# Kernel tuning notes

Measured on AMD Instinct MI355X. Metric: run time of the kernel, lower is better.

Reference implementation:

```python
import jax, jax.numpy as jnp
import numpy as np

MARGIN = 0.3
EPS = 1e-6      # torch F.pairwise_distance eps used inside TripletMarginLoss
BIG = 1000000.0  # same sentinel as original code


def setup_inputs() -> dict:
    key = jax.random.key(0)
    k1, k2 = jax.random.split(key)
    embeddings = jax.random.normal(k1, (4096, 2048), dtype=jnp.float32)
    labels = jax.random.randint(k2, (4096,), 0, 128)  # 128 identities -> ~32 samples each
    return {"embeddings": embeddings, "labels": labels}


def _batch_hard_triplet_loss(emb, labels):
    B = emb.shape[0]
    # pairwise euclidean distances (torch.cdist p=2)
    sq = jnp.sum(emb * emb, axis=1)                      # [B]
    d2 = sq[:, None] + sq[None, :] - 2.0 * (emb @ emb.T)  # [B,B]
    dists = jnp.sqrt(jnp.maximum(d2, 0.0))

    same = labels[:, None] == labels[None, :]            # [B,B] bool
    eye = jnp.eye(B, dtype=bool)
    pos_mask = same & ~eye

    # hard positive: argmax over same-label (self set to -1, others-with-diff-label masked to 0*d -> use -1 uniformly for non-positives, matching dists*mask_pos with diag=-1 since dists>=0)
    pos_d = jnp.where(pos_mask, dists, -1.0)
    hard_pos = jnp.argmax(pos_d, axis=1)                 # [B]
    # hard negative: argmin over different-label (same-label gets +1e6 like original)
    neg_d = jnp.where(same, dists + BIG, dists)
    hard_neg = jnp.argmin(neg_d, axis=1)                 # [B]

    # valid anchors: at least one positive (other than self) and one negative
    valid = (jnp.sum(pos_mask, axis=1) > 0) & (jnp.sum(~same, axis=1) > 0)

    # TripletMarginLoss recomputes distances with eps added to the difference
    dp = jnp.linalg.norm(emb - emb[hard_pos] + EPS, axis=1)
    dn = jnp.linalg.norm(emb - emb[hard_neg] + EPS, axis=1)
    per = jnp.maximum(dp - dn + MARGIN, 0.0)

    cnt = jnp.sum(valid)
    total = jnp.sum(jnp.where(valid, per, 0.0))
    return jnp.where(cnt > 0, total / jnp.maximum(cnt, 1).astype(per.dtype), 0.0)


def reference(embeddings, labels):
    return _batch_hard_triplet_loss(embeddings, labels)
```

## Files before the change

### kernel.cpp

```cpp
#include <hip/hip_runtime.h>
#include <stdint.h>

#define B 4096
#define D 2048
#define BK 128
#define NITER (D / BK)
#define BM 64
#define BN 128

typedef unsigned long long ull;
typedef float f32x4 __attribute__((ext_vector_type(4)));
typedef long v2l __attribute__((ext_vector_type(2)));

#define SENT_P 0x00000000FFFFFFFFull
#define SENT_N (~0ull)

__device__ __forceinline__ void async_copy16(const unsigned char* g, unsigned char* l) {
  __builtin_amdgcn_global_load_lds(
      (const __attribute__((address_space(1))) unsigned int*)g,
      (__attribute__((address_space(3))) unsigned int*)l,
      16, 0, 0);
}

__global__ void k_convert_sq(const float* __restrict__ emb,
                             unsigned char* __restrict__ embq,
                             float* __restrict__ sq,
                             float* __restrict__ rs,
                             ull* __restrict__ bp,
                             ull* __restrict__ bn) {
  const int row = blockIdx.x, t = threadIdx.x;
  const float4* src = (const float4*)(emb + (size_t)row * D);
  float4 v0 = src[2 * t], v1 = src[2 * t + 1];
  float s = v0.x * v0.x + v0.y * v0.y + v0.z * v0.z + v0.w * v0.w
          + v1.x * v1.x + v1.y * v1.y + v1.z * v1.z + v1.w * v1.w;
  float sm = v0.x + v0.y + v0.z + v0.w + v1.x + v1.y + v1.z + v1.w;

  unsigned w0 = __builtin_amdgcn_cvt_pk_fp8_f32(v0.x, v0.y, 0, false);
  w0 = __builtin_amdgcn_cvt_pk_fp8_f32(v0.z, v0.w, w0, true);
  unsigned w1 = __builtin_amdgcn_cvt_pk_fp8_f32(v1.x, v1.y, 0, false);
  w1 = __builtin_amdgcn_cvt_pk_fp8_f32(v1.z, v1.w, w1, true);
  uint2 o; o.x = w0; o.y = w1;
  const int pos = ((t >> 4) << 7) | ((t & 3) << 5) | (((t >> 2) & 3) << 3);
  *(uint2*)(embq + (size_t)row * D + pos) = o;

  for (int off = 32; off; off >>= 1) {
    s  += __shfl_down(s, off, 64);
    sm += __shfl_down(sm, off, 64);
  }
  __shared__ float ps[4], pm[4];
  int lane = t & 63, wave = t >> 6;
  if (lane == 0) { ps[wave] = s; pm[wave] = sm; }
  __syncthreads();
  if (t == 0) {
    sq[row] = ps[0] + ps[1] + ps[2] + ps[3];
    rs[row] = pm[0] + pm[1] + pm[2] + pm[3];
    bp[row] = SENT_P;
    bn[row] = SENT_N;
  }
}

__launch_bounds__(256, 4)
__global__ void k_gemm_select(const unsigned char* __restrict__ embq,
                              const float* __restrict__ sq,
                              const int* __restrict__ labels,
                              ull* __restrict__ best_pos,
                              ull* __restrict__ best_neg) {
  __shared__ __align__(16) unsigned char ldsA[BM * BK];
  __shared__ __align__(16) unsigned char ldsB[BN * BK];

  int rem = blockIdx.x, p = 0;
  while (rem >= 2 * (32 - p)) { rem -= 2 * (32 - p); ++p; }
  int by = 2 * p;
  int c = 32 - p;
  if (rem >= c) { by += 1; rem -= c; }
  const int bx = p + rem;

  const int tid  = threadIdx.x;
  const int lane = tid & 63;
  const int wave = tid >> 6;
  const int wm = wave >> 1, wn = wave & 1;
  const int q = lane >> 4, m15 = lane & 15;
  const int ibase = by * BM, jbase = bx * BN;

  int aoff[2][2], boff[2][4];
#pragma unroll
  for (int sh = 0; sh < 2; ++sh) {
#pragma unroll
    for (int g = 0; g < 2; ++g) {
      int ra = wm * 32 + g * 16 + m15;
      aoff[sh][g] = ra * BK + (((q * 2 + sh) ^ (ra & 7)) * 16);
    }
#pragma unroll
    for (int g = 0; g < 4; ++g) {
      int rb = wn * 64 + g * 16 + m15;
      boff[sh][g] = rb * BK + (((q * 2 + sh) ^ (rb & 7)) * 16);
    }
  }

  const int srow = lane >> 3;
  const int slot = lane & 7;
  size_t agoff[2], bgoff[4];
  int lasta[2], lastb[4];
#pragma unroll
  for (int pp = 0; pp < 2; ++pp) {
    int r0  = wave * 16 + pp * 8;
    int row = r0 + srow;
    agoff[pp] = (size_t)(ibase + row) * D + (slot ^ (row & 7)) * 16;
    lasta[pp] = r0 * BK;
  }
#pragma unroll
  for (int pp = 0; pp < 4; ++pp) {
    int r0  = wave * 32 + pp * 8;
    int row = r0 + srow;
    bgoff[pp] = (size_t)(jbase + row) * D + (slot ^ (row & 7)) * 16;
    lastb[pp] = r0 * BK;
  }

  f32x4 acc[2][4];
  const f32x4 z = {0.f, 0.f, 0.f, 0.f};
#pragma unroll
  for (int a = 0; a < 2; ++a)
#pragma unroll
    for (int b = 0; b < 4; ++b) acc[a][b] = z;

  for (int kb = 0; kb < D; kb += BK) {
    __syncthreads();
#pragma unroll
    for (int pp = 0; pp < 2; ++pp)
      async_copy16(embq + agoff[pp] + kb, &ldsA[lasta[pp]]);
#pragma unroll
    for (int pp = 0; pp < 4; ++pp)
      async_copy16(embq + bgoff[pp] + kb, &ldsB[lastb[pp]]);
    __syncthreads();

#pragma unroll
    for (int sh = 0; sh < 2; ++sh) {
      v2l af[2], bf[4];
#pragma unroll
      for (int g = 0; g < 2; ++g) af[g] = *(const v2l*)&ldsA[aoff[sh][g]];
#pragma unroll
      for (int g = 0; g < 4; ++g) bf[g] = *(const v2l*)&ldsB[boff[sh][g]];
#pragma unroll
      for (int mi = 0; mi < 2; ++mi)
#pragma unroll
        for (int ni = 0; ni < 4; ++ni)
          acc[mi][ni] = __builtin_amdgcn_mfma_f32_16x16x32_fp8_fp8(
              af[mi][0], bf[ni][0], acc[mi][ni], 0, 0, 0);
#pragma unroll
      for (int mi = 0; mi < 2; ++mi)
#pragma unroll
        for (int ni = 0; ni < 4; ++ni)
          acc[mi][ni] = __builtin_amdgcn_mfma_f32_16x16x32_fp8_fp8(
              af[mi][1], bf[ni][1], acc[mi][ni], 0, 0, 0);
    }
  }

  float sqj[4];
  int labj[4];
#pragma unroll
  for (int ni = 0; ni < 4; ++ni) {
    int jj = jbase + wn * 64 + ni * 16 + m15;
    sqj[ni] = sq[jj];
    labj[ni] = labels[jj];
  }

  ull colBp[4], colBn[4];
#pragma unroll
  for (int ni = 0; ni < 4; ++ni) { colBp[ni] = SENT_P; colBn[ni] = SENT_N; }

#pragma unroll
  for (int mi = 0; mi < 2; ++mi) {
#pragma unroll
    for (int r = 0; r < 4; ++r) {
      const int i = ibase + wm * 32 + mi * 16 + q * 4 + r;
      const float si = sq[i];
      const int li = labels[i];
      ull bp = SENT_P;
      ull bn = SENT_N;
#pragma unroll
      for (int ni = 0; ni < 4; ++ni) {
        int jj = jbase + wn * 64 + ni * 16 + m15;
        if (jj > i) {
          float dot = acc[mi][ni][r];
          float d2 = si + sqj[ni] - 2.0f * dot;
          float dist = sqrtf(fmaxf(d2, 0.0f));
          ull pv = ((ull)__float_as_uint(dist)) << 32;
          if (labj[ni] == li) {
            ull cr = pv | (unsigned)(~jj);
            bp = bp > cr ? bp : cr;
            ull cc = pv | (unsigned)(~i);
            colBp[ni] = colBp[ni] > cc ? colBp[ni] : cc;
          } else {
            ull cr = pv | (unsigned)jj;
            bn = bn < cr ? bn : cr;
            ull cc = pv | (unsigned)i;
            colBn[ni] = colBn[ni] < cc ? colBn[ni] : cc;
          }
        }
      }
#pragma unroll
      for (int off = 1; off <= 8; off <<= 1) {
        ull op = __shfl_xor(bp, off, 64);
        ull on = __shfl_xor(bn, off, 64);
        bp = bp > op ? bp : op;
        bn = bn < on ? bn : on;
      }
      if (m15 == 0) {
        if (bp != SENT_P) atomicMax(&best_pos[i], bp);
        if (bn != SENT_N) atomicMin(&best_neg[i], bn);
      }
    }
  }

#pragma unroll
  for (int ni = 0; ni < 4; ++ni) {
    ull cp = colBp[ni], cn = colBn[ni];
#pragma unroll
    for (int off = 16; off <= 32; off <<= 1) {
      ull op = __shfl_xor(cp, off, 64);
      ull on = __shfl_xor(cn, off, 64);
      cp = cp > op ? cp : op;
      cn = cn < on ? cn : on;
    }
    if (q == 0) {
      int j = jbase + wn * 64 + ni * 16 + m15;
      if (cp != SENT_P) atomicMax(&best_pos[j], cp);
      if (cn != SENT_N) atomicMin(&best_neg[j], cn);
    }
  }
}

__global__ void k_loss_final(const ull* __restrict__ best_pos,
                             const ull* __restrict__ best_neg,
                             const float* __restrict__ rs,
                             float* __restrict__ out) {
  float per = 0.0f;
  int v = 0;
  for (int i = threadIdx.x; i < B; i += 1024) {
    ull bp = best_pos[i], bn = best_neg[i];
    if (bp != SENT_P && bn != SENT_N) {
      unsigned pRaw = ~(unsigned)bp;
      unsigned nRaw = (unsigned)bn;
      int pi = pRaw < (unsigned)B ? (int)pRaw : 0;
      int ni = nRaw < (unsigned)B ? (int)nRaw : 0;
      float distp = __uint_as_float((unsigned)(bp >> 32));
      float distn = __uint_as_float((unsigned)(bn >> 32));
      float ri = rs[i];
      const float e = 1e-6f, de2 = (float)D * 1e-12f;
      float dp2 = distp * distp + 2.0f * e * (ri - rs[pi]) + de2;
      float dn2 = distn * distn + 2.0f * e * (ri - rs[ni]) + de2;
      float dp = sqrtf(fmaxf(dp2, 0.0f));
      float dn = sqrtf(fmaxf(dn2, 0.0f));
      per += fmaxf(dp - dn + 0.3f, 0.0f);
      v += 1;
    }
  }
  for (int off = 32; off; off >>= 1) {
    per += __shfl_down(per, off, 64);
    v   += __shfl_down(v, off, 64);
  }
  __shared__ float pps[16];
  __shared__ int pvs[16];
  int lane = threadIdx.x & 63, wave = threadIdx.x >> 6;
  if (lane == 0) { pps[wave] = per; pvs[wave] = v; }
  __syncthreads();
  if (threadIdx.x == 0) {
    float t = 0.f;
    int cv = 0;
#pragma unroll
    for (int w = 0; w < 16; ++w) { t += pps[w]; cv += pvs[w]; }
    out[0] = cv > 0 ? t / (float)cv : 0.0f;
  }
}

extern "C" void kernel_launch(void* const* d_in, const int* in_sizes, int n_in,
                              void* d_out, int out_size, void* d_ws, size_t ws_size,
                              hipStream_t stream) {
  const float* emb = (const float*)d_in[0];
  const int* labels = (const int*)d_in[1];
  float* out = (float*)d_out;
  char* ws = (char*)d_ws;

  const size_t off_embq = 0;
  const size_t off_sq   = off_embq + (size_t)B * D;
  const size_t off_rs   = off_sq + (size_t)B * 4;
  const size_t off_bp   = off_rs + (size_t)B * 4;
  const size_t off_bn   = off_bp + (size_t)B * 8;

  unsigned char* embq = (unsigned char*)(ws + off_embq);
  float* sq   = (float*)(ws + off_sq);
  float* rs   = (float*)(ws + off_rs);
  ull* bp     = (ull*)(ws + off_bp);
  ull* bn     = (ull*)(ws + off_bn);

  hipLaunchKernelGGL(k_convert_sq, dim3(B), dim3(256), 0, stream,
                     emb, embq, sq, rs, bp, bn);
  hipLaunchKernelGGL(k_gemm_select, dim3(1056), dim3(256), 0, stream,
                     embq, sq, labels, bp, bn);
  hipLaunchKernelGGL(k_loss_final, dim3(1), dim3(1024), 0, stream,
                     bp, bn, rs, out);
}
```

Baseline: 122.1 us.

## Halve GEMM block to two waves with 64x64 warp tiles; parallelize final reduction

The GEMM/select kernel now runs 128 threads (2 waves) per block instead of 4. Each wave computes a 64x64 sub-tile with 16 accumulators, which raises MFMA work per LDS fragment load and cuts per-block scheduling overhead, at the cost of more registers and fewer waves to hide latency. The final loss kernel moves from a single 1024-thread block to 16 blocks. These combine partial sums through global atomics and a last-block-done counter, and the counters are zeroed in the convert kernel.

```diff
diff --git a/kernel.cpp b/kernel.cpp
--- a/kernel.cpp
+++ b/kernel.cpp
@@ -27,7 +27,10 @@
                              float* __restrict__ sq,
                              float* __restrict__ rs,
                              ull* __restrict__ bp,
-                             ull* __restrict__ bn) {
+                             ull* __restrict__ bn,
+                             float* __restrict__ red_sum,
+                             int* __restrict__ red_cnt,
+                             int* __restrict__ red_done) {
   const int row = blockIdx.x, t = threadIdx.x;
   const float4* src = (const float4*)(emb + (size_t)row * D);
   float4 v0 = src[2 * t], v1 = src[2 * t + 1];
@@ -56,10 +59,11 @@
     rs[row] = pm[0] + pm[1] + pm[2] + pm[3];
     bp[row] = SENT_P;
     bn[row] = SENT_N;
-  }
-}
-
-__launch_bounds__(256, 4)
+    if (row == 0) { *red_sum = 0.0f; *red_cnt = 0; *red_done = 0; }
+  }
+}
+
+__launch_bounds__(128, 3)
 __global__ void k_gemm_select(const unsigned char* __restrict__ embq,
                               const float* __restrict__ sq,
                               const int* __restrict__ labels,
@@ -78,76 +82,72 @@
   const int tid  = threadIdx.x;
   const int lane = tid & 63;
   const int wave = tid >> 6;
-  const int wm = wave >> 1, wn = wave & 1;
   const int q = lane >> 4, m15 = lane & 15;
   const int ibase = by * BM, jbase = bx * BN;
 
-  int aoff[2][2], boff[2][4];
+  int aoff[2][4], boff[2][4];
 #pragma unroll
   for (int sh = 0; sh < 2; ++sh) {
 #pragma unroll
-    for (int g = 0; g < 2; ++g) {
-      int ra = wm * 32 + g * 16 + m15;
+    for (int g = 0; g < 4; ++g) {
+      int ra = g * 16 + m15;
       aoff[sh][g] = ra * BK + (((q * 2 + sh) ^ (ra & 7)) * 16);
-    }
-#pragma unroll
-    for (int g = 0; g < 4; ++g) {
-      int rb = wn * 64 + g * 16 + m15;
+      int rb = wave * 64 + g * 16 + m15;
       boff[sh][g] = rb * BK + (((q * 2 + sh) ^ (rb & 7)) * 16);
     }
   }
 
   const int srow = lane >> 3;
   const int slot = lane & 7;
-  size_t agoff[2], bgoff[4];
-  int lasta[2], lastb[4];
-#pragma unroll
-  for (int pp = 0; pp < 2; ++pp) {
-    int r0  = wave * 16 + pp * 8;
+  size_t agoff[4], bgoff[8];
+  int lasta[4], lastb[8];
+#pragma unroll
+  for (int pp = 0; pp < 4; ++pp) {
+    int r0  = wave * 32 + pp * 8;
     int row = r0 + srow;
     agoff[pp] = (size_t)(ibase + row) * D + (slot ^ (row & 7)) * 16;
     lasta[pp] = r0 * BK;
   }
 #pragma unroll
-  for (int pp = 0; pp < 4; ++pp) {
-    int r0  = wave * 32 + pp * 8;
+  for (int pp = 0; pp < 8; ++pp) {
+    int r0  = wave * 64 + pp * 8;
     int row = r0 + srow;
     bgoff[pp] = (size_t)(jbase + row) * D + (slot ^ (row & 7)) * 16;
     lastb[pp] = r0 * BK;
   }
 
-  f32x4 acc[2][4];
+  f32x4 acc[4][4];
   const f32x4 z = {0.f, 0.f, 0.f, 0.f};
 #pragma unroll
-  for (int a = 0; a < 2; ++a)
+  for (int a = 0; a < 4; ++a)
 #pragma unroll
     for (int b = 0; b < 4; ++b) acc[a][b] = z;
 
   for (int kb = 0; kb < D; kb += BK) {
     __syncthreads();
 #pragma unroll
-    for (int pp = 0; pp < 2; ++pp)
+    for (int pp = 0; pp < 4; ++pp)
       async_copy16(embq + agoff[pp] + kb, &ldsA[lasta[pp]]);
 #pragma unroll
-    for (int pp = 0; pp < 4; ++pp)
+    for (int pp = 0; pp < 8; ++pp)
       async_copy16(embq + bgoff[pp] + kb, &ldsB[lastb[pp]]);
     __syncthreads();
 
 #pragma unroll
     for (int sh = 0; sh < 2; ++sh) {
-      v2l af[2], bf[4];
-#pragma unroll
-      for (int g = 0; g < 2; ++g) af[g] = *(const v2l*)&ldsA[aoff[sh][g]];
+      v2l af[4], bf[4];
+#pragma unroll
+      for (int g = 0; g < 4; ++g) af[g] = *(const v2l*)&ldsA[aoff[sh][g]];
 #pragma unroll
       for (int g = 0; g < 4; ++g) bf[g] = *(const v2l*)&ldsB[boff[sh][g]];
 #pragma unroll
-      for (int mi = 0; mi < 2; ++mi)
+      for (int mi = 0; mi < 4; ++mi)
 #pragma unroll
         for (int ni = 0; ni < 4; ++ni)
           acc[mi][ni] = __builtin_amdgcn_mfma_f32_16x16x32_fp8_fp8(
               af[mi][0], bf[ni][0], acc[mi][ni], 0, 0, 0);
 #pragma unroll
-      for (int mi = 0; mi < 2; ++mi)
+      for (int mi = 0; mi < 4; ++mi)
 #pragma unroll
         for (int ni = 0; ni < 4; ++ni)
           acc[mi][ni] = __builtin_amdgcn_mfma_f32_16x16x32_fp8_fp8(
@@ -159,7 +159,7 @@
   int labj[4];
 #pragma unroll
   for (int ni = 0; ni < 4; ++ni) {
-    int jj = jbase + wn * 64 + ni * 16 + m15;
+    int jj = jbase + wave * 64 + ni * 16 + m15;
     sqj[ni] = sq[jj];
     labj[ni] = labels[jj];
   }
@@ -169,17 +169,17 @@
   for (int ni = 0; ni < 4; ++ni) { colBp[ni] = SENT_P; colBn[ni] = SENT_N; }
 
 #pragma unroll
-  for (int mi = 0; mi < 2; ++mi) {
+  for (int mi = 0; mi < 4; ++mi) {
 #pragma unroll
     for (int r = 0; r < 4; ++r) {
-      const int i = ibase + wm * 32 + mi * 16 + q * 4 + r;
+      const int i = ibase + mi * 16 + q * 4 + r;
       const float si = sq[i];
       const int li = labels[i];
       ull bp = SENT_P;
       ull bn = SENT_N;
 #pragma unroll
       for (int ni = 0; ni < 4; ++ni) {
-        int jj = jbase + wn * 64 + ni * 16 + m15;
+        int jj = jbase + wave * 64 + ni * 16 + m15;
         if (jj > i) {
           float dot = acc[mi][ni][r];
           float d2 = si + sqj[ni] - 2.0f * dot;
@@ -223,7 +223,7 @@
       cn = cn < on ? cn : on;
     }
     if (q == 0) {
-      int j = jbase + wn * 64 + ni * 16 + m15;
+      int j = jbase + wave * 64 + ni * 16 + m15;
       if (cp != SENT_P) atomicMax(&best_pos[j], cp);
       if (cn != SENT_N) atomicMin(&best_neg[j], cn);
     }
@@ -233,43 +233,51 @@
 __global__ void k_loss_final(const ull* __restrict__ best_pos,
                              const ull* __restrict__ best_neg,
                              const float* __restrict__ rs,
+                             float* __restrict__ red_sum,
+                             int* __restrict__ red_cnt,
+                             int* __restrict__ red_done,
                              float* __restrict__ out) {
+  const int i = blockIdx.x * 256 + threadIdx.x;
   float per = 0.0f;
   int v = 0;
-  for (int i = threadIdx.x; i < B; i += 1024) {
-    ull bp = best_pos[i], bn = best_neg[i];
-    if (bp != SENT_P && bn != SENT_N) {
-      unsigned pRaw = ~(unsigned)bp;
-      unsigned nRaw = (unsigned)bn;
-      int pi = pRaw < (unsigned)B ? (int)pRaw : 0;
-      int ni = nRaw < (unsigned)B ? (int)nRaw : 0;
-      float distp = __uint_as_float((unsigned)(bp >> 32));
-      float distn = __uint_as_float((unsigned)(bn >> 32));
-      float ri = rs[i];
-      const float e = 1e-6f, de2 = (float)D * 1e-12f;
-      float dp2 = distp * distp + 2.0f * e * (ri - rs[pi]) + de2;
-      float dn2 = distn * distn + 2.0f * e * (ri - rs[ni]) + de2;
-      float dp = sqrtf(fmaxf(dp2, 0.0f));
-      float dn = sqrtf(fmaxf(dn2, 0.0f));
-      per += fmaxf(dp - dn + 0.3f, 0.0f);
-      v += 1;
-    }
+  ull bp = best_pos[i], bn = best_neg[i];
+  if (bp != SENT_P && bn != SENT_N) {
+    unsigned pRaw = ~(unsigned)bp;
+    unsigned nRaw = (unsigned)bn;
+    int pi = pRaw < (unsigned)B ? (int)pRaw : 0;
+    int ni = nRaw < (unsigned)B ? (int)nRaw : 0;
+    float distp = __uint_as_float((unsigned)(bp >> 32));
+    float distn = __uint_as_float((unsigned)(bn >> 32));
+    float ri = rs[i];
+    const float e = 1e-6f, de2 = (float)D * 1e-12f;
+    float dp2 = distp * distp + 2.0f * e * (ri - rs[pi]) + de2;
+    float dn2 = distn * distn + 2.0f * e * (ri - rs[ni]) + de2;
+    float dp = sqrtf(fmaxf(dp2, 0.0f));
+    float dn = sqrtf(fmaxf(dn2, 0.0f));
+    per = fmaxf(dp - dn + 0.3f, 0.0f);
+    v = 1;
   }
   for (int off = 32; off; off >>= 1) {
     per += __shfl_down(per, off, 64);
     v   += __shfl_down(v, off, 64);
   }
-  __shared__ float pps[16];
-  __shared__ int pvs[16];
+  __shared__ float pps[4];
+  __shared__ int pvs[4];
   int lane = threadIdx.x & 63, wave = threadIdx.x >> 6;
   if (lane == 0) { pps[wave] = per; pvs[wave] = v; }
   __syncthreads();
   if (threadIdx.x == 0) {
-    float t = 0.f;
-    int cv = 0;
-#pragma unroll
-    for (int w = 0; w < 16; ++w) { t += pps[w]; cv += pvs[w]; }
-    out[0] = cv > 0 ? t / (float)cv : 0.0f;
+    float t = pps[0] + pps[1] + pps[2] + pps[3];
+    int cv = pvs[0] + pvs[1] + pvs[2] + pvs[3];
+    atomicAdd(red_sum, t);
+    atomicAdd(red_cnt, cv);
+    __threadfence();
+    int old = atomicAdd(red_done, 1);
+    if (old == (int)gridDim.x - 1) {
+      float s = atomicAdd(red_sum, 0.0f);
+      int cc = atomicAdd(red_cnt, 0);
+      out[0] = cc > 0 ? s / (float)cc : 0.0f;
+    }
   }
 }
 
@@ -286,17 +294,21 @@
   const size_t off_rs   = off_sq + (size_t)B * 4;
   const size_t off_bp   = off_rs + (size_t)B * 4;
   const size_t off_bn   = off_bp + (size_t)B * 8;
+  const size_t off_red  = off_bn + (size_t)B * 8;
 
   unsigned char* embq = (unsigned char*)(ws + off_embq);
   float* sq   = (float*)(ws + off_sq);
   float* rs   = (float*)(ws + off_rs);
   ull* bp     = (ull*)(ws + off_bp);
   ull* bn     = (ull*)(ws + off_bn);
+  float* red_sum = (float*)(ws + off_red);
+  int* red_cnt   = (int*)(ws + off_red + 4);
+  int* red_done  = (int*)(ws + off_red + 8);
 
   hipLaunchKernelGGL(k_convert_sq, dim3(B), dim3(256), 0, stream,
-                     emb, embq, sq, rs, bp, bn);
-  hipLaunchKernelGGL(k_gemm_select, dim3(1056), dim3(256), 0, stream,
+                     emb, embq, sq, rs, bp, bn, red_sum, red_cnt, red_done);
+  hipLaunchKernelGGL(k_gemm_select, dim3(1056), dim3(128), 0, stream,
                      embq, sq, labels, bp, bn);
-  hipLaunchKernelGGL(k_loss_final, dim3(1), dim3(1024), 0, stream,
-                     bp, bn, rs, out);
-}
+  hipLaunchKernelGGL(k_loss_final, dim3(B / 256), dim3(256), 0, stream,
+                     bp, bn, rs, red_sum, red_cnt, red_done, out);
+}
```

Measured after the change: 129.6 us. 1.06x slower.
